# Kernel optimization log

Hardware: AMD Instinct MI355X
Metric: run time of the kernel (lower is better)

## Reference

```python
import jax, jax.numpy as jnp
import numpy as np

H = 256           # hidden_size
D_IN = 4 * H      # 1024
D_K = 8 * H       # 2048
B, N = 8, 2048


def setup_inputs() -> dict:
    key = jax.random.key(0)
    ks = jax.random.split(key, 7)
    s_in = 1.0 / np.sqrt(D_IN)
    s_dk = 1.0 / np.sqrt(D_K)
    x = jax.random.normal(ks[0], (B, N, D_IN), dtype=jnp.float32)
    Wq = jax.random.uniform(ks[1], (D_IN, D_K), jnp.float32, -s_in, s_in)
    Wk = jax.random.uniform(ks[2], (D_IN, D_K), jnp.float32, -s_in, s_in)
    Wv = jax.random.uniform(ks[3], (D_IN, D_K), jnp.float32, -s_in, s_in)
    Wfc = jax.random.uniform(ks[4], (D_K, D_IN), jnp.float32, -s_dk, s_dk)
    bfc = jax.random.uniform(ks[5], (D_IN,), jnp.float32, -s_dk, s_dk)
    gamma = jnp.ones((D_IN,), jnp.float32)
    beta = jnp.zeros((D_IN,), jnp.float32)
    return {"x": x, "Wq": Wq, "Wk": Wk, "Wv": Wv, "Wfc": Wfc,
            "bfc": bfc, "gamma": gamma, "beta": beta}


def layer_norm(y, gamma, beta, eps=1e-5):
    mu = jnp.mean(y, axis=-1, keepdims=True)
    var = jnp.var(y, axis=-1, keepdims=True)
    return (y - mu) * jax.lax.rsqrt(var + eps) * gamma + beta


def reference(x, Wq, Wk, Wv, Wfc, bfc, gamma, beta):
    # Q/K/V projections: [B, N, D_K]
    q = jnp.einsum('bnd,dk->bnk', x, Wq)
    k = jnp.einsum('bnd,dk->bnk', x, Wk)
    v = jnp.einsum('bnd,dk->bnk', x, Wv)
    # NOTE: original module has NO 1/sqrt(d_k) scaling — keep it faithful.
    scores = jnp.einsum('bnk,bmk->bnm', q, k)           # [B, N, N]
    attn = jax.nn.softmax(scores, axis=-1)
    att_x = jnp.einsum('bnm,bmk->bnk', attn, v)          # [B, N, D_K]
    h = jax.nn.relu(jnp.einsum('bnk,kd->bnd', att_x, Wfc) + bfc)
    return layer_norm(x + h, gamma, beta)
```

## Files before the change

### kernel.cpp

```cpp
#include <hip/hip_runtime.h>
#include <stdint.h>


#define DEVI __device__ __forceinline__

typedef uint16_t u16;
typedef _Float16 f16x8 __attribute__((ext_vector_type(8)));
typedef float f32x4 __attribute__((ext_vector_type(4)));

DEVI u16 f2h(float f) {
  union { _Float16 h; u16 u; } v;
  v.h = (_Float16)f;
  return v.u;
}

DEVI void gload_lds16(const void* g, void* lds) {
  __builtin_amdgcn_global_load_lds(
      (const __attribute__((address_space(1))) void*)g,
      (__attribute__((address_space(3))) void*)lds, 16, 0, 0);
}

template <int EPI>
__global__ __launch_bounds__(512, 2) void gemm256(
    const u16* __restrict__ A, const u16* __restrict__ B, void* __restrict__ C,
    int K, int lda, int ldb, int ldc,
    long aZ, long bZ, long cZ,
    const float* __restrict__ bias, const float* __restrict__ xres)
{
  __shared__ u16 lds[3 * 24576];
  char* ldsB = (char*)lds;
  const int tid = threadIdx.x;
  const int bz = blockIdx.z;

  const int gx = gridDim.x;
  int fl = blockIdx.y * gx + blockIdx.x;
  const int cpx = (gx * gridDim.y) >> 3;
  fl = (fl & 7) * cpx + (fl >> 3);
  const int bx = fl % gx, by = fl / gx;

  const u16* Ab = A + (long)bz * aZ + (long)(by * 256) * lda;
  const u16* Bb = B + (long)bz * bZ + (long)(bx * 128) * ldb;

  long aoff[4], boff[2];
#pragma unroll
  for (int r = 0; r < 4; ++r) {
    const int d = tid * 16 + r * 8192;
    const int dl = d ^ (((d >> 7) & 7) << 4);
    aoff[r] = (long)(dl >> 7) * (lda * 2) + (dl & 127);
  }
#pragma unroll
  for (int r = 0; r < 2; ++r) {
    const int d = tid * 16 + r * 8192;
    const int dl = d ^ (((d >> 7) & 7) << 4);
    boff[r] = (long)(dl >> 7) * (ldb * 2) + (dl & 127);
  }

  const int wid = tid >> 6, lane = tid & 63;
  const int wm = wid >> 1, wn = wid & 1;
  const int l15 = lane & 15;
  const int swzm = (lane & 7) << 4;
  const int ko0 = ((lane >> 4) * 16) ^ swzm;
  const int ko1 = (64 + (lane >> 4) * 16) ^ swzm;
  const int stgD = wid * 1024;

  f32x4 acc[4][4] = {};

  auto STAGE = [&](int t) {
    char* ab = ldsB + (t % 3) * 49152;
    char* bb = ab + 32768;
    const long kB = (long)t * 128;
#pragma unroll
    for (int r = 0; r < 4; ++r)
      gload_lds16((const char*)Ab + aoff[r] + kB, ab + stgD + r * 8192);
#pragma unroll
    for (int r = 0; r < 2; ++r)
      gload_lds16((const char*)Bb + boff[r] + kB, bb + stgD + r * 8192);
  };

  const int NT = K >> 6;
  STAGE(0);
  STAGE(1);

  for (int t = 0; t < NT; ++t) {
    if (t + 1 < NT) {
      asm volatile("s_waitcnt vmcnt(6)" ::: "memory");
    } else {
      asm volatile("s_waitcnt vmcnt(0)" ::: "memory");
    }
    __builtin_amdgcn_s_barrier();
    if (t + 2 < NT) STAGE(t + 2);

    const char* ab = ldsB + (t % 3) * 49152;
    const char* bb = ab + 32768;
#pragma unroll
    for (int ks = 0; ks < 2; ++ks) {
      const int ko = ks ? ko1 : ko0;
      f16x8 af[4], bf[4];
#pragma unroll
      for (int m = 0; m < 4; ++m)
        af[m] = *(const f16x8*)(ab + (wm * 64 + m * 16 + l15) * 128 + ko);
#pragma unroll
      for (int n = 0; n < 4; ++n)
        bf[n] = *(const f16x8*)(bb + (wn * 64 + n * 16 + l15) * 128 + ko);
      __builtin_amdgcn_s_setprio(1);
#pragma unroll
      for (int m = 0; m < 4; ++m)
#pragma unroll
        for (int n = 0; n < 4; ++n)
          acc[m][n] = __builtin_amdgcn_mfma_f32_16x16x32_f16(af[m], bf[n], acc[m][n], 0, 0, 0);
      __builtin_amdgcn_s_setprio(0);
    }
  }

  const long cBase = (long)bz * cZ;
  const int rowBase = by * 256 + wm * 64;
  const int colBase = bx * 128 + wn * 64;

  if constexpr (EPI == 3) {
    u16* vT = (u16*)C;
#pragma unroll
    for (int m = 0; m < 4; ++m) {
      const long row0 = rowBase + m * 16 + (lane >> 4) * 4;
      const long bb2 = (row0 >> 11) * 4194304L + (row0 & 2047);
#pragma unroll
      for (int n = 0; n < 4; ++n) {
        const int col = colBase + n * 16 + l15;
        ushort4 h;
        h.x = f2h(acc[m][n][0]); h.y = f2h(acc[m][n][1]);
        h.z = f2h(acc[m][n][2]); h.w = f2h(acc[m][n][3]);
        *(ushort4*)(vT + bb2 + (long)col * 2048) = h;
      }
    }
  } else {
#pragma unroll
    for (int m = 0; m < 4; ++m) {
#pragma unroll
      for (int r = 0; r < 4; ++r) {
        const long row = rowBase + m * 16 + (lane >> 4) * 4 + r;
#pragma unroll
        for (int n = 0; n < 4; ++n) {
          const int col = colBase + n * 16 + l15;
          float v = acc[m][n][r];
          if constexpr (EPI == 0) {
            ((u16*)C)[cBase + row * ldc + col] = f2h(v);
          } else if constexpr (EPI == 1) {
            ((float*)C)[cBase + row * ldc + col] = v;
          } else {
            v += bias[col];
            v = fmaxf(v, 0.0f);
            v += xres[row * (long)ldc + col];
            ((float*)C)[row * (long)ldc + col] = v;
          }
        }
      }
    }
  }
}

template <int EPI>
__global__ __launch_bounds__(256) void gemm_bt(
    const u16* __restrict__ A, const u16* __restrict__ B, void* __restrict__ C,
    int K, int lda, int ldb, int ldc,
    long aZ, long bZ, long cZ,
    const float* __restrict__ bias, const float* __restrict__ xres)
{
  __shared__ u16 sA[128 * 32];
  __shared__ u16 sB[128 * 32];
  const int tid = threadIdx.x;
  const int bz = blockIdx.z;
  const u16* Ab = A + (long)bz * aZ + (long)(blockIdx.y * 128) * lda;
  const u16* Bb = B + (long)bz * bZ + (long)(blockIdx.x * 128) * ldb;

  const int lane = tid & 63;
  const int wr = (tid >> 7) & 1;
  const int wc = (tid >> 6) & 1;
  const int l15 = lane & 15, l4 = lane >> 4;

  const int f0 = tid, f1 = tid + 256;
  const long ga0 = (long)(f0 >> 2) * lda + (f0 & 3) * 8;
  const long ga1 = (long)(f1 >> 2) * lda + (f1 & 3) * 8;
  const long gb0 = (long)(f0 >> 2) * ldb + (f0 & 3) * 8;
  const long gb1 = (long)(f1 >> 2) * ldb + (f1 & 3) * 8;
  u16* sAd0 = sA + (tid & ~63) * 8;
  u16* sAd1 = sA + 2048 + (tid & ~63) * 8;
  u16* sBd0 = sB + (tid & ~63) * 8;
  u16* sBd1 = sB + 2048 + (tid & ~63) * 8;

  f32x4 acc[4][4] = {};

  for (int k0 = 0; k0 < K; k0 += 32) {
    gload_lds16(Ab + ga0 + k0, sAd0);
    gload_lds16(Ab + ga1 + k0, sAd1);
    gload_lds16(Bb + gb0 + k0, sBd0);
    gload_lds16(Bb + gb1 + k0, sBd1);
    __syncthreads();
    f16x8 af[4], bf[4];
#pragma unroll
    for (int m = 0; m < 4; ++m)
      af[m] = *(const f16x8*)(sA + (wr * 64 + m * 16 + l15) * 32 + l4 * 8);
#pragma unroll
    for (int n = 0; n < 4; ++n)
      bf[n] = *(const f16x8*)(sB + (wc * 64 + n * 16 + l15) * 32 + l4 * 8);
#pragma unroll
    for (int m = 0; m < 4; ++m)
#pragma unroll
      for (int n = 0; n < 4; ++n)
        acc[m][n] = __builtin_amdgcn_mfma_f32_16x16x32_f16(af[m], bf[n], acc[m][n], 0, 0, 0);
    __syncthreads();
  }

  const long cBase = (long)bz * cZ;
  const int rowBase = blockIdx.y * 128 + wr * 64;
  const int colBase = blockIdx.x * 128 + wc * 64;

  if constexpr (EPI == 3) {
    u16* vT = (u16*)C;
#pragma unroll
    for (int m = 0; m < 4; ++m) {
      const long row0 = rowBase + m * 16 + l4 * 4;
      const long bb = (row0 >> 11) * 4194304L + (row0 & 2047);
#pragma unroll
      for (int n = 0; n < 4; ++n) {
        const int col = colBase + n * 16 + l15;
        ushort4 h;
        h.x = f2h(acc[m][n][0]); h.y = f2h(acc[m][n][1]);
        h.z = f2h(acc[m][n][2]); h.w = f2h(acc[m][n][3]);
        *(ushort4*)(vT + bb + (long)col * 2048) = h;
      }
    }
  } else {
#pragma unroll
    for (int m = 0; m < 4; ++m) {
#pragma unroll
      for (int r = 0; r < 4; ++r) {
        const long row = rowBase + m * 16 + l4 * 4 + r;
#pragma unroll
        for (int n = 0; n < 4; ++n) {
          const int col = colBase + n * 16 + l15;
          float v = acc[m][n][r];
          if constexpr (EPI == 0) {
            ((u16*)C)[cBase + row * ldc + col] = f2h(v);
          } else if constexpr (EPI == 1) {
            ((float*)C)[cBase + row * ldc + col] = v;
          } else {
            v += bias[col];
            v = fmaxf(v, 0.0f);
            v += xres[row * (long)ldc + col];
            ((float*)C)[row * (long)ldc + col] = v;
          }
        }
      }
    }
  }
}

__global__ __launch_bounds__(256) void softmax_rows(float* __restrict__ scores)
{
  const long row = blockIdx.x;
  const float* src = scores + row * 2048;
  const int tid = threadIdx.x;
  float4 a = ((const float4*)src)[tid];
  float4 b = ((const float4*)src)[tid + 256];
  float m = fmaxf(fmaxf(fmaxf(a.x, a.y), fmaxf(a.z, a.w)),
                  fmaxf(fmaxf(b.x, b.y), fmaxf(b.z, b.w)));
#pragma unroll
  for (int o = 32; o; o >>= 1) m = fmaxf(m, __shfl_xor(m, o));
  __shared__ float redm[4];
  if ((tid & 63) == 0) redm[tid >> 6] = m;
  __syncthreads();
  m = fmaxf(fmaxf(redm[0], redm[1]), fmaxf(redm[2], redm[3]));

  float e[8];
  e[0] = __expf(a.x - m); e[1] = __expf(a.y - m);
  e[2] = __expf(a.z - m); e[3] = __expf(a.w - m);
  e[4] = __expf(b.x - m); e[5] = __expf(b.y - m);
  e[6] = __expf(b.z - m); e[7] = __expf(b.w - m);
  float s = ((e[0] + e[1]) + (e[2] + e[3])) + ((e[4] + e[5]) + (e[6] + e[7]));
#pragma unroll
  for (int o = 32; o; o >>= 1) s += __shfl_xor(s, o);
  __shared__ float reds[4];
  if ((tid & 63) == 0) reds[tid >> 6] = s;
  __syncthreads();
  s = (reds[0] + reds[1]) + (reds[2] + reds[3]);
  const float inv = 1.0f / s;

  u16* dst = (u16*)scores + row * 4096;
  uint2 w0, w1;
  w0.x = (uint32_t)f2h(e[0] * inv) | ((uint32_t)f2h(e[1] * inv) << 16);
  w0.y = (uint32_t)f2h(e[2] * inv) | ((uint32_t)f2h(e[3] * inv) << 16);
  w1.x = (uint32_t)f2h(e[4] * inv) | ((uint32_t)f2h(e[5] * inv) << 16);
  w1.y = (uint32_t)f2h(e[6] * inv) | ((uint32_t)f2h(e[7] * inv) << 16);
  ((uint2*)dst)[tid] = w0;
  ((uint2*)dst)[tid + 256] = w1;
}

__global__ __launch_bounds__(256) void layernorm_rows(
    const float* __restrict__ y, const float* __restrict__ gamma,
    const float* __restrict__ beta, float* __restrict__ out)
{
  const long row = blockIdx.x;
  const int tid = threadIdx.x;
  float4 v = ((const float4*)(y + row * 1024))[tid];
  float s = (v.x + v.y) + (v.z + v.w);
  float q = (v.x * v.x + v.y * v.y) + (v.z * v.z + v.w * v.w);
#pragma unroll
  for (int o = 32; o; o >>= 1) { s += __shfl_xor(s, o); q += __shfl_xor(q, o); }
  __shared__ float rs[4], rq[4];
  if ((tid & 63) == 0) { rs[tid >> 6] = s; rq[tid >> 6] = q; }
  __syncthreads();
  s = (rs[0] + rs[1]) + (rs[2] + rs[3]);
  q = (rq[0] + rq[1]) + (rq[2] + rq[3]);
  const float mu = s * (1.0f / 1024.0f);
  const float var = q * (1.0f / 1024.0f) - mu * mu;
  const float rstd = rsqrtf(var + 1e-5f);
  float4 g = ((const float4*)gamma)[tid];
  float4 be = ((const float4*)beta)[tid];
  float4 o;
  o.x = (v.x - mu) * rstd * g.x + be.x;
  o.y = (v.y - mu) * rstd * g.y + be.y;
  o.z = (v.z - mu) * rstd * g.z + be.z;
  o.w = (v.w - mu) * rstd * g.w + be.w;
  __syncthreads();
  ((float4*)(out + row * 1024))[tid] = o;
}

__global__ __launch_bounds__(256) void cvt_f32_f16(
    const float* __restrict__ in, u16* __restrict__ out, long n4)
{
  const long stride = (long)gridDim.x * 256;
  for (long i = (long)blockIdx.x * 256 + threadIdx.x; i < n4; i += stride) {
    float4 v = ((const float4*)in)[i];
    uint2 p;
    p.x = (uint32_t)f2h(v.x) | ((uint32_t)f2h(v.y) << 16);
    p.y = (uint32_t)f2h(v.z) | ((uint32_t)f2h(v.w) << 16);
    ((uint2*)out)[i] = p;
  }
}

__global__ __launch_bounds__(256) void tw_f32(
    const float* __restrict__ in, u16* __restrict__ out, int R, int C)
{
  __shared__ float T[32][33];
  const int c0 = blockIdx.x * 32, r0 = blockIdx.y * 32;
  const int tx = threadIdx.x & 31, ty = threadIdx.x >> 5;
#pragma unroll
  for (int i = 0; i < 4; ++i)
    T[ty + i * 8][tx] = in[(long)(r0 + ty + i * 8) * C + c0 + tx];
  __syncthreads();
#pragma unroll
  for (int i = 0; i < 4; ++i)
    out[(long)(c0 + ty + i * 8) * R + r0 + tx] = f2h(T[tx][ty + i * 8]);
}

__global__ __launch_bounds__(256) void transpose_u16(
    const u16* __restrict__ in, u16* __restrict__ out, int R, int C)
{
  __shared__ u16 T[32][33];
  const long zo = (long)blockIdx.z * R * C;
  const int c0 = blockIdx.x * 32, r0 = blockIdx.y * 32;
  const int tx = threadIdx.x & 31, ty = threadIdx.x >> 5;
#pragma unroll
  for (int i = 0; i < 4; ++i)
    T[ty + i * 8][tx] = in[zo + (long)(r0 + ty + i * 8) * C + c0 + tx];
  __syncthreads();
#pragma unroll
  for (int i = 0; i < 4; ++i)
    out[zo + (long)(c0 + ty + i * 8) * R + r0 + tx] = T[tx][ty + i * 8];
}

extern "C" void kernel_launch(void* const* d_in, const int* in_sizes, int n_in,
                              void* d_out, int out_size, void* d_ws, size_t ws_size,
                              hipStream_t stream)
{
  const float* x     = (const float*)d_in[0];
  const float* Wq    = (const float*)d_in[1];
  const float* Wk    = (const float*)d_in[2];
  const float* Wv    = (const float*)d_in[3];
  const float* Wfc   = (const float*)d_in[4];
  const float* bfc   = (const float*)d_in[5];
  const float* gamma = (const float*)d_in[6];
  const float* beta  = (const float*)d_in[7];
  float* out = (float*)d_out;

  char* ws = (char*)d_ws;

  u16* wqkvT = (u16*)(ws + 0);
  u16* wfcT  = (u16*)(ws + 12582912);
  tw_f32<<<dim3(64, 32), 256, 0, stream>>>(Wq, wqkvT, 1024, 2048);
  tw_f32<<<dim3(64, 32), 256, 0, stream>>>(Wk, wqkvT + (long)2048 * 1024, 1024, 2048);
  tw_f32<<<dim3(64, 32), 256, 0, stream>>>(Wv, wqkvT + (long)2 * 2048 * 1024, 1024, 2048);
  tw_f32<<<dim3(32, 64), 256, 0, stream>>>(Wfc, wfcT, 2048, 1024);

  if (ws_size >= 251658240ULL) {
    u16*  q_  = (u16*)(ws + 16777216);
    u16*  k_  = (u16*)(ws + 83886080);
    u16*  vT  = (u16*)(ws + 150994944);
    float* sc = (float*)(ws + 218103808);
    u16*  xb  = (u16*)sc;

    cvt_f32_f16<<<2048, 256, 0, stream>>>(x, xb, (long)16384 * 1024 / 4);

    gemm256<0><<<dim3(16, 64, 2), 512, 0, stream>>>(
        xb, wqkvT, (void*)q_, 1024, 1024, 1024, 2048,
        0L, (long)2048 * 1024, (long)16384 * 2048, nullptr, nullptr);
    gemm256<3><<<dim3(16, 64, 1), 512, 0, stream>>>(
        xb, wqkvT + (long)2 * 2048 * 1024, (void*)vT, 1024, 1024, 1024, 2048,
        0L, 0L, 0L, nullptr, nullptr);

    for (int c = 0; c < 4; ++c) {
      const u16* qc = q_ + (long)c * 512 * 2048;
      gemm256<1><<<dim3(16, 2, 8), 512, 0, stream>>>(
          qc, k_, (void*)sc, 2048, 2048, 2048, 2048,
          (long)2048 * 2048, (long)2048 * 2048, (long)512 * 2048, nullptr, nullptr);
      softmax_rows<<<4096, 256, 0, stream>>>(sc);
      gemm256<0><<<dim3(16, 2, 8), 512, 0, stream>>>(
          (const u16*)sc, vT, (void*)(q_ + (long)c * 512 * 2048), 2048, 4096, 2048, 2048,
          (long)512 * 4096, (long)2048 * 2048, (long)2048 * 2048, nullptr, nullptr);
    }

    gemm256<2><<<dim3(8, 64, 1), 512, 0, stream>>>(
        q_, wfcT, (void*)out, 2048, 2048, 2048, 1024,
        0L, 0L, 0L, bfc, x);
  } else if (ws_size >= 109051904ULL) {
    u16*  xb2 = (u16*)(ws + 16777216);
    u16*  q2  = (u16*)(ws + 25165824);
    u16*  k2  = q2 + (long)2 * 2048 * 2048;
    u16*  v2  = q2 + (long)4 * 2048 * 2048;
    float* sc2 = (float*)(ws + 75497472);
    u16*  vT2   = k2;
    u16*  attx2 = q2;

    for (int p = 0; p < 4; ++p) {
      const float* xp = x + (long)p * 4096 * 1024;
      cvt_f32_f16<<<1024, 256, 0, stream>>>(xp, xb2, (long)4096 * 1024 / 4);
      for (int b = 0; b < 2; ++b)
        gemm_bt<0><<<dim3(16, 16, 3), 256, 0, stream>>>(
            xb2 + (long)b * 2048 * 1024, wqkvT, (void*)(q2 + (long)b * 2048 * 2048),
            1024, 1024, 1024, 2048,
            0L, (long)2048 * 1024, (long)2 * 2048 * 2048, nullptr, nullptr);
      gemm_bt<1><<<dim3(16, 16, 2), 256, 0, stream>>>(
          q2, k2, (void*)sc2, 2048, 2048, 2048, 2048,
          (long)2048 * 2048, (long)2048 * 2048, (long)2048 * 2048, nullptr, nullptr);
      softmax_rows<<<4096, 256, 0, stream>>>(sc2);
      transpose_u16<<<dim3(64, 64, 2), 256, 0, stream>>>(v2, vT2, 2048, 2048);
      gemm_bt<0><<<dim3(16, 16, 2), 256, 0, stream>>>(
          (const u16*)sc2, vT2, (void*)attx2, 2048, 4096, 2048, 2048,
          (long)2048 * 4096, (long)2048 * 2048, (long)2048 * 2048, nullptr, nullptr);
      gemm_bt<2><<<dim3(8, 32, 1), 256, 0, stream>>>(
          attx2, wfcT, (void*)(out + (long)p * 4096 * 1024), 2048, 2048, 2048, 1024,
          0L, 0L, 0L, bfc, xp);
    }
  } else {
    u16*  xb_b   = (u16*)(ws + 16777216);
    u16*  qkv_b  = (u16*)(ws + 20971520);
    u16*  q_b    = qkv_b;
    u16*  k_b    = qkv_b + (long)2048 * 2048;
    u16*  v_b    = qkv_b + (long)2 * 2048 * 2048;
    float* sc_b  = (float*)(ws + 46137344);
    u16*  vT_b   = k_b;
    u16*  attx_b = q_b;

    for (int b = 0; b < 8; ++b) {
      const float* x_b = x + (long)b * 2048 * 1024;
      cvt_f32_f16<<<512, 256, 0, stream>>>(x_b, xb_b, (long)2048 * 1024 / 4);
      gemm_bt<0><<<dim3(16, 16, 3), 256, 0, stream>>>(
          xb_b, wqkvT, (void*)qkv_b, 1024, 1024, 1024, 2048,
          0L, (long)2048 * 1024, (long)2048 * 2048, nullptr, nullptr);
      gemm_bt<1><<<dim3(16, 16, 1), 256, 0, stream>>>(
          q_b, k_b, (void*)sc_b, 2048, 2048, 2048, 2048,
          0L, 0L, 0L, nullptr, nullptr);
      softmax_rows<<<2048, 256, 0, stream>>>(sc_b);
      transpose_u16<<<dim3(64, 64, 1), 256, 0, stream>>>(v_b, vT_b, 2048, 2048);
      gemm_bt<0><<<dim3(16, 16, 1), 256, 0, stream>>>(
          (const u16*)sc_b, vT_b, (void*)attx_b, 2048, 4096, 2048, 2048,
          0L, 0L, 0L, nullptr, nullptr);
      gemm_bt<2><<<dim3(8, 16, 1), 256, 0, stream>>>(
          attx_b, wfcT, (void*)(out + (long)b * 2048 * 1024), 2048, 2048, 2048, 1024,
          0L, 0L, 0L, bfc, x_b);
    }
  }

  layernorm_rows<<<16384, 256, 0, stream>>>(out, gamma, beta, out);
}
```

Baseline: 710.2 us.

## Add 256x256-tile GEMM kernel for QKV and output projections

Introduces a new GEMM kernel with a 256x256 output tile per 512-thread block, 8x4 MFMA fragments per wave and double-buffered LDS staging, replacing the 256x128 tile kernel for the Q/K/V projections and the final FC+bias+relu+residual projection. The larger tile doubles arithmetic intensity per loaded byte and halves global traffic for the weight operand. The 256x128 kernel is kept for the attention GEMMs with its epilogue simplified. The trade-off is higher register pressure from 128 accumulator floats per thread, a shallower two-stage pipeline instead of three, and half as many blocks in flight.

```diff
diff --git a/kernel.cpp b/kernel.cpp
--- a/kernel.cpp
+++ b/kernel.cpp
@@ -21,11 +21,140 @@
 }
 
 template <int EPI>
-__global__ __launch_bounds__(512, 2) void gemm256(
+__global__ __launch_bounds__(512, 2) void gemm512(
     const u16* __restrict__ A, const u16* __restrict__ B, void* __restrict__ C,
     int K, int lda, int ldb, int ldc,
     long aZ, long bZ, long cZ,
     const float* __restrict__ bias, const float* __restrict__ xres)
+{
+  __shared__ u16 lds[2 * 32768];
+  char* ldsB = (char*)lds;
+  const int tid = threadIdx.x;
+  const int bz = blockIdx.z;
+
+  const int gx = gridDim.x;
+  int fl = blockIdx.y * gx + blockIdx.x;
+  const int cpx = (gx * gridDim.y) >> 3;
+  fl = (fl & 7) * cpx + (fl >> 3);
+  const int bx = fl % gx, by = fl / gx;
+
+  const u16* Ab = A + (long)bz * aZ + (long)(by * 256) * lda;
+  const u16* Bb = B + (long)bz * bZ + (long)(bx * 256) * ldb;
+
+  long aoff[4], boff[4];
+#pragma unroll
+  for (int r = 0; r < 4; ++r) {
+    const int d = tid * 16 + r * 8192;
+    const int dl = d ^ (((d >> 7) & 7) << 4);
+    aoff[r] = (long)(dl >> 7) * (lda * 2) + (dl & 127);
+    boff[r] = (long)(dl >> 7) * (ldb * 2) + (dl & 127);
+  }
+
+  const int wid = tid >> 6, lane = tid & 63;
+  const int wm = wid >> 2, wn = wid & 3;
+  const int l15 = lane & 15;
+  const int swzm = (lane & 7) << 4;
+  const int ko0 = ((lane >> 4) * 16) ^ swzm;
+  const int ko1 = (64 + (lane >> 4) * 16) ^ swzm;
+  const int stgD = wid * 1024;
+
+  f32x4 acc[8][4] = {};
+
+  auto STAGE = [&](int t) {
+    char* ab = ldsB + (t & 1) * 65536;
+    char* bb = ab + 32768;
+    const long kB = (long)t * 128;
+#pragma unroll
+    for (int r = 0; r < 4; ++r)
+      gload_lds16((const char*)Ab + aoff[r] + kB, ab + stgD + r * 8192);
+#pragma unroll
+    for (int r = 0; r < 4; ++r)
+      gload_lds16((const char*)Bb + boff[r] + kB, bb + stgD + r * 8192);
+  };
+
+  const int NT = K >> 6;
+  STAGE(0);
+
+  for (int t = 0; t < NT; ++t) {
+    if (t + 1 < NT) {
+      STAGE(t + 1);
+      asm volatile("s_waitcnt vmcnt(8)" ::: "memory");
+    } else {
+      asm volatile("s_waitcnt vmcnt(0)" ::: "memory");
+    }
+    __builtin_amdgcn_s_barrier();
+
+    const char* ab = ldsB + (t & 1) * 65536;
+    const char* bb = ab + 32768;
+#pragma unroll
+    for (int ks = 0; ks < 2; ++ks) {
+      const int ko = ks ? ko1 : ko0;
+      f16x8 af[8], bf[4];
+#pragma unroll
+      for (int m = 0; m < 8; ++m)
+        af[m] = *(const f16x8*)(ab + (wm * 128 + m * 16 + l15) * 128 + ko);
+#pragma unroll
+      for (int n = 0; n < 4; ++n)
+        bf[n] = *(const f16x8*)(bb + (wn * 64 + n * 16 + l15) * 128 + ko);
+      __builtin_amdgcn_s_setprio(1);
+#pragma unroll
+      for (int m = 0; m < 8; ++m)
+#pragma unroll
+        for (int n = 0; n < 4; ++n)
+          acc[m][n] = __builtin_amdgcn_mfma_f32_16x16x32_f16(af[m], bf[n], acc[m][n], 0, 0, 0);
+      __builtin_amdgcn_s_setprio(0);
+    }
+    __builtin_amdgcn_s_barrier();
+  }
+
+  const long cBase = (long)bz * cZ;
+  const int rowBase = by * 256 + wm * 128;
+  const int colBase = bx * 256 + wn * 64;
+
+  if constexpr (EPI == 3) {
+    u16* vT = (u16*)C;
+#pragma unroll
+    for (int m = 0; m < 8; ++m) {
+      const long row0 = rowBase + m * 16 + (lane >> 4) * 4;
+      const long bb2 = (row0 >> 11) * 4194304L + (row0 & 2047);
+#pragma unroll
+      for (int n = 0; n < 4; ++n) {
+        const int col = colBase + n * 16 + l15;
+        ushort4 h;
+        h.x = f2h(acc[m][n][0]); h.y = f2h(acc[m][n][1]);
+        h.z = f2h(acc[m][n][2]); h.w = f2h(acc[m][n][3]);
+        *(ushort4*)(vT + bb2 + (long)col * 2048) = h;
+      }
+    }
+  } else {
+#pragma unroll
+    for (int m = 0; m < 8; ++m) {
+#pragma unroll
+      for (int r = 0; r < 4; ++r) {
+        const long row = rowBase + m * 16 + (lane >> 4) * 4 + r;
+#pragma unroll
+        for (int n = 0; n < 4; ++n) {
+          const int col = colBase + n * 16 + l15;
+          float v = acc[m][n][r];
+          if constexpr (EPI == 0) {
+            ((u16*)C)[cBase + row * ldc + col] = f2h(v);
+          } else {
+            v += bias[col];
+            v = fmaxf(v, 0.0f);
+            v += xres[row * (long)ldc + col];
+            ((float*)C)[row * (long)ldc + col] = v;
+          }
+        }
+      }
+    }
+  }
+}
+
+template <int EPI>
+__global__ __launch_bounds__(512, 2) void gemm256(
+    const u16* __restrict__ A, const u16* __restrict__ B, void* __restrict__ C,
+    int K, int lda, int ldb, int ldc,
+    long aZ, long bZ, long cZ)
 {
   __shared__ u16 lds[3 * 24576];
   char* ldsB = (char*)lds;
@@ -115,42 +244,19 @@
   const long cBase = (long)bz * cZ;
   const int rowBase = by * 256 + wm * 64;
   const int colBase = bx * 128 + wn * 64;
-
-  if constexpr (EPI == 3) {
-    u16* vT = (u16*)C;
-#pragma unroll
-    for (int m = 0; m < 4; ++m) {
-      const long row0 = rowBase + m * 16 + (lane >> 4) * 4;
-      const long bb2 = (row0 >> 11) * 4194304L + (row0 & 2047);
+#pragma unroll
+  for (int m = 0; m < 4; ++m) {
+#pragma unroll
+    for (int r = 0; r < 4; ++r) {
+      const long row = rowBase + m * 16 + (lane >> 4) * 4 + r;
 #pragma unroll
       for (int n = 0; n < 4; ++n) {
         const int col = colBase + n * 16 + l15;
-        ushort4 h;
-        h.x = f2h(acc[m][n][0]); h.y = f2h(acc[m][n][1]);
-        h.z = f2h(acc[m][n][2]); h.w = f2h(acc[m][n][3]);
-        *(ushort4*)(vT + bb2 + (long)col * 2048) = h;
-      }
-    }
-  } else {
-#pragma unroll
-    for (int m = 0; m < 4; ++m) {
-#pragma unroll
-      for (int r = 0; r < 4; ++r) {
-        const long row = rowBase + m * 16 + (lane >> 4) * 4 + r;
-#pragma unroll
-        for (int n = 0; n < 4; ++n) {
-          const int col = colBase + n * 16 + l15;
-          float v = acc[m][n][r];
-          if constexpr (EPI == 0) {
-            ((u16*)C)[cBase + row * ldc + col] = f2h(v);
-          } else if constexpr (EPI == 1) {
-            ((float*)C)[cBase + row * ldc + col] = v;
-          } else {
-            v += bias[col];
-            v = fmaxf(v, 0.0f);
-            v += xres[row * (long)ldc + col];
-            ((float*)C)[row * (long)ldc + col] = v;
-          }
+        float v = acc[m][n][r];
+        if constexpr (EPI == 0) {
+          ((u16*)C)[cBase + row * ldc + col] = f2h(v);
+        } else {
+          ((float*)C)[cBase + row * ldc + col] = v;
         }
       }
     }
@@ -400,10 +506,10 @@
 
     cvt_f32_f16<<<2048, 256, 0, stream>>>(x, xb, (long)16384 * 1024 / 4);
 
-    gemm256<0><<<dim3(16, 64, 2), 512, 0, stream>>>(
+    gemm512<0><<<dim3(8, 64, 2), 512, 0, stream>>>(
         xb, wqkvT, (void*)q_, 1024, 1024, 1024, 2048,
         0L, (long)2048 * 1024, (long)16384 * 2048, nullptr, nullptr);
-    gemm256<3><<<dim3(16, 64, 1), 512, 0, stream>>>(
+    gemm512<3><<<dim3(8, 64, 1), 512, 0, stream>>>(
         xb, wqkvT + (long)2 * 2048 * 1024, (void*)vT, 1024, 1024, 1024, 2048,
         0L, 0L, 0L, nullptr, nullptr);
 
@@ -411,14 +517,14 @@
       const u16* qc = q_ + (long)c * 512 * 2048;
       gemm256<1><<<dim3(16, 2, 8), 512, 0, stream>>>(
           qc, k_, (void*)sc, 2048, 2048, 2048, 2048,
-          (long)2048 * 2048, (long)2048 * 2048, (long)512 * 2048, nullptr, nullptr);
+          (long)2048 * 2048, (long)2048 * 2048, (long)512 * 2048);
       softmax_rows<<<4096, 256, 0, stream>>>(sc);
       gemm256<0><<<dim3(16, 2, 8), 512, 0, stream>>>(
           (const u16*)sc, vT, (void*)(q_ + (long)c * 512 * 2048), 2048, 4096, 2048, 2048,
-          (long)512 * 4096, (long)2048 * 2048, (long)2048 * 2048, nullptr, nullptr);
-    }
-
-    gemm256<2><<<dim3(8, 64, 1), 512, 0, stream>>>(
+          (long)512 * 4096, (long)2048 * 2048, (long)2048 * 2048);
+    }
+
+    gemm512<2><<<dim3(4, 64, 1), 512, 0, stream>>>(
         q_, wfcT, (void*)out, 2048, 2048, 2048, 1024,
         0L, 0L, 0L, bfc, x);
   } else if (ws_size >= 109051904ULL) {
```

After: 711.2 us. About the same (+0.1%).

## Use 256x256 8-phase GEMM tiles and fp16 attention scores with larger chunks

Applied to the files above, without the earlier changes.

Replaces the 256x128 triple-buffered GEMM with a 256x256 tile kernel that double-buffers LDS and interleaves four quarter-tile loads between MFMA phases, raising arithmetic intensity per block. Attention scores are now stored in fp16 instead of fp32, and softmax reads and writes fp16 in place, which halves score traffic and lets chunks cover 1024 query rows instead of 512. The cost is fewer blocks per GEMM, more accumulator registers per thread, and some precision loss from storing pre-softmax logits in fp16, which could overflow since there is no 1/sqrt(d) scaling.

```diff
diff --git a/kernel.cpp b/kernel.cpp
--- a/kernel.cpp
+++ b/kernel.cpp
@@ -13,6 +13,11 @@
   v.h = (_Float16)f;
   return v.u;
 }
+DEVI float h2f(u16 x) {
+  union { _Float16 h; u16 u; } v;
+  v.u = x;
+  return (float)v.h;
+}
 
 DEVI void gload_lds16(const void* g, void* lds) {
   __builtin_amdgcn_global_load_lds(
@@ -21,13 +26,13 @@
 }
 
 template <int EPI>
-__global__ __launch_bounds__(512, 2) void gemm256(
+__global__ __launch_bounds__(512, 2) void gemm8p(
     const u16* __restrict__ A, const u16* __restrict__ B, void* __restrict__ C,
     int K, int lda, int ldb, int ldc,
     long aZ, long bZ, long cZ,
     const float* __restrict__ bias, const float* __restrict__ xres)
 {
-  __shared__ u16 lds[3 * 24576];
+  __shared__ u16 lds[2 * 32768];
   char* ldsB = (char*)lds;
   const int tid = threadIdx.x;
   const int bz = blockIdx.z;
@@ -39,87 +44,154 @@
   const int bx = fl % gx, by = fl / gx;
 
   const u16* Ab = A + (long)bz * aZ + (long)(by * 256) * lda;
-  const u16* Bb = B + (long)bz * bZ + (long)(bx * 128) * ldb;
-
-  long aoff[4], boff[2];
-#pragma unroll
-  for (int r = 0; r < 4; ++r) {
-    const int d = tid * 16 + r * 8192;
-    const int dl = d ^ (((d >> 7) & 7) << 4);
-    aoff[r] = (long)(dl >> 7) * (lda * 2) + (dl & 127);
-  }
-#pragma unroll
-  for (int r = 0; r < 2; ++r) {
-    const int d = tid * 16 + r * 8192;
-    const int dl = d ^ (((d >> 7) & 7) << 4);
-    boff[r] = (long)(dl >> 7) * (ldb * 2) + (dl & 127);
-  }
+  const u16* Bb = B + (long)bz * bZ + (long)(bx * 256) * ldb;
 
   const int wid = tid >> 6, lane = tid & 63;
-  const int wm = wid >> 1, wn = wid & 1;
+  const int wm = wid >> 2, wn = wid & 3;
   const int l15 = lane & 15;
-  const int swzm = (lane & 7) << 4;
-  const int ko0 = ((lane >> 4) * 16) ^ swzm;
-  const int ko1 = (64 + (lane >> 4) * 16) ^ swzm;
-  const int stgD = wid * 1024;
-
-  f32x4 acc[4][4] = {};
-
-  auto STAGE = [&](int t) {
-    char* ab = ldsB + (t % 3) * 49152;
-    char* bb = ab + 32768;
+
+  int aBase[2][2]; long aoff[2][2];
+  int bBase[2][2]; long boff[2][2];
+#pragma unroll
+  for (int h = 0; h < 2; ++h) {
+#pragma unroll
+    for (int j = 0; j < 2; ++j) {
+      const int s = wid * 2 + j;
+      int rs = (s < 8) ? (64 * h + s * 8) : (128 + 64 * h + (s - 8) * 8);
+      aBase[h][j] = rs * 128;
+      {
+        const int d = rs * 128 + lane * 16;
+        const int dl = d ^ (((d >> 7) & 7) << 4);
+        aoff[h][j] = (long)(dl >> 7) * (lda * 2) + (dl & 127);
+      }
+      rs = 64 * (s >> 2) + 32 * h + (s & 3) * 8;
+      bBase[h][j] = 32768 + rs * 128;
+      {
+        const int d = rs * 128 + lane * 16;
+        const int dl = d ^ (((d >> 7) & 7) << 4);
+        boff[h][j] = (long)(dl >> 7) * (ldb * 2) + (dl & 127);
+      }
+    }
+  }
+
+  const int swz = (lane & 7) << 4;
+  const int ko0 = ((lane >> 4) * 16) ^ swz;
+  const int ko1 = (64 + (lane >> 4) * 16) ^ swz;
+
+  f32x4 acc[8][4] = {};
+
+  auto STAGE_A = [&](int t, int h) {
+    char* dst = ldsB + (t & 1) * 65536;
     const long kB = (long)t * 128;
 #pragma unroll
-    for (int r = 0; r < 4; ++r)
-      gload_lds16((const char*)Ab + aoff[r] + kB, ab + stgD + r * 8192);
-#pragma unroll
-    for (int r = 0; r < 2; ++r)
-      gload_lds16((const char*)Bb + boff[r] + kB, bb + stgD + r * 8192);
+    for (int j = 0; j < 2; ++j)
+      gload_lds16((const char*)Ab + aoff[h][j] + kB, dst + aBase[h][j]);
   };
+  auto STAGE_B = [&](int t, int h) {
+    char* dst = ldsB + (t & 1) * 65536;
+    const long kB = (long)t * 128;
+#pragma unroll
+    for (int j = 0; j < 2; ++j)
+      gload_lds16((const char*)Bb + boff[h][j] + kB, dst + bBase[h][j]);
+  };
 
   const int NT = K >> 6;
-  STAGE(0);
-  STAGE(1);
+  STAGE_A(0, 0); STAGE_B(0, 0); STAGE_B(0, 1); STAGE_A(0, 1);
 
   for (int t = 0; t < NT; ++t) {
-    if (t + 1 < NT) {
-      asm volatile("s_waitcnt vmcnt(6)" ::: "memory");
-    } else {
-      asm volatile("s_waitcnt vmcnt(0)" ::: "memory");
-    }
+    const bool more = (t + 1 < NT);
+    const char* ab = ldsB + (t & 1) * 65536;
+    const char* bb = ab + 32768;
+    f16x8 af[8], bf0[4], bf1[4];
+
+    asm volatile("s_waitcnt vmcnt(4)" ::: "memory");
     __builtin_amdgcn_s_barrier();
-    if (t + 2 < NT) STAGE(t + 2);
-
-    const char* ab = ldsB + (t % 3) * 49152;
-    const char* bb = ab + 32768;
-#pragma unroll
-    for (int ks = 0; ks < 2; ++ks) {
-      const int ko = ks ? ko1 : ko0;
-      f16x8 af[4], bf[4];
+    if (more) STAGE_A(t + 1, 0);
+#pragma unroll
+    for (int m = 0; m < 4; ++m) {
+      const char* r = ab + (wm * 128 + m * 16 + l15) * 128;
+      af[2 * m] = *(const f16x8*)(r + ko0);
+      af[2 * m + 1] = *(const f16x8*)(r + ko1);
+    }
+#pragma unroll
+    for (int n = 0; n < 2; ++n) {
+      const char* r = bb + (wn * 64 + n * 16 + l15) * 128;
+      bf0[2 * n] = *(const f16x8*)(r + ko0);
+      bf0[2 * n + 1] = *(const f16x8*)(r + ko1);
+    }
+    __builtin_amdgcn_s_setprio(1);
+#pragma unroll
+    for (int ks = 0; ks < 2; ++ks)
 #pragma unroll
       for (int m = 0; m < 4; ++m)
-        af[m] = *(const f16x8*)(ab + (wm * 64 + m * 16 + l15) * 128 + ko);
-#pragma unroll
-      for (int n = 0; n < 4; ++n)
-        bf[n] = *(const f16x8*)(bb + (wn * 64 + n * 16 + l15) * 128 + ko);
-      __builtin_amdgcn_s_setprio(1);
+#pragma unroll
+        for (int n = 0; n < 2; ++n)
+          acc[m][n] = __builtin_amdgcn_mfma_f32_16x16x32_f16(
+              af[2 * m + ks], bf0[2 * n + ks], acc[m][n], 0, 0, 0);
+    __builtin_amdgcn_s_setprio(0);
+
+    if (more) asm volatile("s_waitcnt vmcnt(4)" ::: "memory");
+    else      asm volatile("s_waitcnt vmcnt(2)" ::: "memory");
+    __builtin_amdgcn_s_barrier();
+    if (more) STAGE_B(t + 1, 0);
+#pragma unroll
+    for (int n = 0; n < 2; ++n) {
+      const char* r = bb + (wn * 64 + (n + 2) * 16 + l15) * 128;
+      bf1[2 * n] = *(const f16x8*)(r + ko0);
+      bf1[2 * n + 1] = *(const f16x8*)(r + ko1);
+    }
+    __builtin_amdgcn_s_setprio(1);
+#pragma unroll
+    for (int ks = 0; ks < 2; ++ks)
 #pragma unroll
       for (int m = 0; m < 4; ++m)
 #pragma unroll
-        for (int n = 0; n < 4; ++n)
-          acc[m][n] = __builtin_amdgcn_mfma_f32_16x16x32_f16(af[m], bf[n], acc[m][n], 0, 0, 0);
-      __builtin_amdgcn_s_setprio(0);
-    }
+        for (int n = 0; n < 2; ++n)
+          acc[m][n + 2] = __builtin_amdgcn_mfma_f32_16x16x32_f16(
+              af[2 * m + ks], bf1[2 * n + ks], acc[m][n + 2], 0, 0, 0);
+    __builtin_amdgcn_s_setprio(0);
+
+    if (more) asm volatile("s_waitcnt vmcnt(4)" ::: "memory");
+    else      asm volatile("s_waitcnt vmcnt(0)" ::: "memory");
+    __builtin_amdgcn_s_barrier();
+    if (more) STAGE_B(t + 1, 1);
+#pragma unroll
+    for (int m = 0; m < 4; ++m) {
+      const char* r = ab + (wm * 128 + (m + 4) * 16 + l15) * 128;
+      af[2 * m] = *(const f16x8*)(r + ko0);
+      af[2 * m + 1] = *(const f16x8*)(r + ko1);
+    }
+    __builtin_amdgcn_s_setprio(1);
+#pragma unroll
+    for (int ks = 0; ks < 2; ++ks)
+#pragma unroll
+      for (int m = 0; m < 4; ++m)
+#pragma unroll
+        for (int n = 0; n < 2; ++n)
+          acc[m + 4][n] = __builtin_amdgcn_mfma_f32_16x16x32_f16(
+              af[2 * m + ks], bf0[2 * n + ks], acc[m + 4][n], 0, 0, 0);
+    __builtin_amdgcn_s_setprio(0);
+    if (more) STAGE_A(t + 1, 1);
+    __builtin_amdgcn_s_setprio(1);
+#pragma unroll
+    for (int ks = 0; ks < 2; ++ks)
+#pragma unroll
+      for (int m = 0; m < 4; ++m)
+#pragma unroll
+        for (int n = 0; n < 2; ++n)
+          acc[m + 4][n + 2] = __builtin_amdgcn_mfma_f32_16x16x32_f16(
+              af[2 * m + ks], bf1[2 * n + ks], acc[m + 4][n + 2], 0, 0, 0);
+    __builtin_amdgcn_s_setprio(0);
   }
 
   const long cBase = (long)bz * cZ;
-  const int rowBase = by * 256 + wm * 64;
-  const int colBase = bx * 128 + wn * 64;
+  const int rowBase = by * 256 + wm * 128;
+  const int colBase = bx * 256 + wn * 64;
 
   if constexpr (EPI == 3) {
     u16* vT = (u16*)C;
 #pragma unroll
-    for (int m = 0; m < 4; ++m) {
+    for (int m = 0; m < 8; ++m) {
       const long row0 = rowBase + m * 16 + (lane >> 4) * 4;
       const long bb2 = (row0 >> 11) * 4194304L + (row0 & 2047);
 #pragma unroll
@@ -133,7 +205,7 @@
     }
   } else {
 #pragma unroll
-    for (int m = 0; m < 4; ++m) {
+    for (int m = 0; m < 8; ++m) {
 #pragma unroll
       for (int r = 0; r < 4; ++r) {
         const long row = rowBase + m * 16 + (lane >> 4) * 4 + r;
@@ -143,8 +215,6 @@
           float v = acc[m][n][r];
           if constexpr (EPI == 0) {
             ((u16*)C)[cBase + row * ldc + col] = f2h(v);
-          } else if constexpr (EPI == 1) {
-            ((float*)C)[cBase + row * ldc + col] = v;
           } else {
             v += bias[col];
             v = fmaxf(v, 0.0f);
@@ -213,45 +283,67 @@
   const int rowBase = blockIdx.y * 128 + wr * 64;
   const int colBase = blockIdx.x * 128 + wc * 64;
 
-  if constexpr (EPI == 3) {
-    u16* vT = (u16*)C;
-#pragma unroll
-    for (int m = 0; m < 4; ++m) {
-      const long row0 = rowBase + m * 16 + l4 * 4;
-      const long bb = (row0 >> 11) * 4194304L + (row0 & 2047);
+#pragma unroll
+  for (int m = 0; m < 4; ++m) {
+#pragma unroll
+    for (int r = 0; r < 4; ++r) {
+      const long row = rowBase + m * 16 + l4 * 4 + r;
 #pragma unroll
       for (int n = 0; n < 4; ++n) {
         const int col = colBase + n * 16 + l15;
-        ushort4 h;
-        h.x = f2h(acc[m][n][0]); h.y = f2h(acc[m][n][1]);
-        h.z = f2h(acc[m][n][2]); h.w = f2h(acc[m][n][3]);
-        *(ushort4*)(vT + bb + (long)col * 2048) = h;
-      }
-    }
-  } else {
-#pragma unroll
-    for (int m = 0; m < 4; ++m) {
-#pragma unroll
-      for (int r = 0; r < 4; ++r) {
-        const long row = rowBase + m * 16 + l4 * 4 + r;
-#pragma unroll
-        for (int n = 0; n < 4; ++n) {
-          const int col = colBase + n * 16 + l15;
-          float v = acc[m][n][r];
-          if constexpr (EPI == 0) {
-            ((u16*)C)[cBase + row * ldc + col] = f2h(v);
-          } else if constexpr (EPI == 1) {
-            ((float*)C)[cBase + row * ldc + col] = v;
-          } else {
-            v += bias[col];
-            v = fmaxf(v, 0.0f);
-            v += xres[row * (long)ldc + col];
-            ((float*)C)[row * (long)ldc + col] = v;
-          }
+        float v = acc[m][n][r];
+        if constexpr (EPI == 0) {
+          ((u16*)C)[cBase + row * ldc + col] = f2h(v);
+        } else if constexpr (EPI == 1) {
+          ((float*)C)[cBase + row * ldc + col] = v;
+        } else {
+          v += bias[col];
+          v = fmaxf(v, 0.0f);
+          v += xres[row * (long)ldc + col];
+          ((float*)C)[row * (long)ldc + col] = v;
         }
       }
     }
   }
+}
+
+__global__ __launch_bounds__(256) void softmax_rows16(u16* __restrict__ sc)
+{
+  const long row = blockIdx.x;
+  u16* p = sc + row * 2048;
+  const int tid = threadIdx.x;
+  uint4 w = ((const uint4*)p)[tid];
+  float e[8];
+  e[0] = h2f(w.x & 0xffff); e[1] = h2f(w.x >> 16);
+  e[2] = h2f(w.y & 0xffff); e[3] = h2f(w.y >> 16);
+  e[4] = h2f(w.z & 0xffff); e[5] = h2f(w.z >> 16);
+  e[6] = h2f(w.w & 0xffff); e[7] = h2f(w.w >> 16);
+  float m = fmaxf(fmaxf(fmaxf(e[0], e[1]), fmaxf(e[2], e[3])),
+                  fmaxf(fmaxf(e[4], e[5]), fmaxf(e[6], e[7])));
+#pragma unroll
+  for (int o = 32; o; o >>= 1) m = fmaxf(m, __shfl_xor(m, o));
+  __shared__ float redm[4];
+  if ((tid & 63) == 0) redm[tid >> 6] = m;
+  __syncthreads();
+  m = fmaxf(fmaxf(redm[0], redm[1]), fmaxf(redm[2], redm[3]));
+
+  float s = 0.0f;
+#pragma unroll
+  for (int i = 0; i < 8; ++i) { e[i] = __expf(e[i] - m); s += e[i]; }
+#pragma unroll
+  for (int o = 32; o; o >>= 1) s += __shfl_xor(s, o);
+  __shared__ float reds[4];
+  if ((tid & 63) == 0) reds[tid >> 6] = s;
+  __syncthreads();
+  s = (reds[0] + reds[1]) + (reds[2] + reds[3]);
+  const float inv = 1.0f / s;
+
+  uint4 o;
+  o.x = (uint32_t)f2h(e[0] * inv) | ((uint32_t)f2h(e[1] * inv) << 16);
+  o.y = (uint32_t)f2h(e[2] * inv) | ((uint32_t)f2h(e[3] * inv) << 16);
+  o.z = (uint32_t)f2h(e[4] * inv) | ((uint32_t)f2h(e[5] * inv) << 16);
+  o.w = (uint32_t)f2h(e[6] * inv) | ((uint32_t)f2h(e[7] * inv) << 16);
+  ((uint4*)p)[tid] = o;
 }
 
 __global__ __launch_bounds__(256) void softmax_rows(float* __restrict__ scores)
@@ -392,33 +484,33 @@
   tw_f32<<<dim3(32, 64), 256, 0, stream>>>(Wfc, wfcT, 2048, 1024);
 
   if (ws_size >= 251658240ULL) {
-    u16*  q_  = (u16*)(ws + 16777216);
-    u16*  k_  = (u16*)(ws + 83886080);
-    u16*  vT  = (u16*)(ws + 150994944);
-    float* sc = (float*)(ws + 218103808);
-    u16*  xb  = (u16*)sc;
+    u16*  q_   = (u16*)(ws + 16777216);
+    u16*  k_   = (u16*)(ws + 83886080);
+    u16*  vT   = (u16*)(ws + 150994944);
+    u16*  sc16 = (u16*)(ws + 218103808);
+    u16*  xb   = sc16;
 
     cvt_f32_f16<<<2048, 256, 0, stream>>>(x, xb, (long)16384 * 1024 / 4);
 
-    gemm256<0><<<dim3(16, 64, 2), 512, 0, stream>>>(
+    gemm8p<0><<<dim3(8, 64, 2), 512, 0, stream>>>(
         xb, wqkvT, (void*)q_, 1024, 1024, 1024, 2048,
         0L, (long)2048 * 1024, (long)16384 * 2048, nullptr, nullptr);
-    gemm256<3><<<dim3(16, 64, 1), 512, 0, stream>>>(
+    gemm8p<3><<<dim3(8, 64, 1), 512, 0, stream>>>(
         xb, wqkvT + (long)2 * 2048 * 1024, (void*)vT, 1024, 1024, 1024, 2048,
         0L, 0L, 0L, nullptr, nullptr);
 
-    for (int c = 0; c < 4; ++c) {
-      const u16* qc = q_ + (long)c * 512 * 2048;
-      gemm256<1><<<dim3(16, 2, 8), 512, 0, stream>>>(
-          qc, k_, (void*)sc, 2048, 2048, 2048, 2048,
-          (long)2048 * 2048, (long)2048 * 2048, (long)512 * 2048, nullptr, nullptr);
-      softmax_rows<<<4096, 256, 0, stream>>>(sc);
-      gemm256<0><<<dim3(16, 2, 8), 512, 0, stream>>>(
-          (const u16*)sc, vT, (void*)(q_ + (long)c * 512 * 2048), 2048, 4096, 2048, 2048,
-          (long)512 * 4096, (long)2048 * 2048, (long)2048 * 2048, nullptr, nullptr);
-    }
-
-    gemm256<2><<<dim3(8, 64, 1), 512, 0, stream>>>(
+    for (int c = 0; c < 2; ++c) {
+      const u16* qc = q_ + (long)c * 1024 * 2048;
+      gemm8p<0><<<dim3(8, 4, 8), 512, 0, stream>>>(
+          qc, k_, (void*)sc16, 2048, 2048, 2048, 2048,
+          (long)2048 * 2048, (long)2048 * 2048, (long)1024 * 2048, nullptr, nullptr);
+      softmax_rows16<<<8192, 256, 0, stream>>>(sc16);
+      gemm8p<0><<<dim3(8, 4, 8), 512, 0, stream>>>(
+          sc16, vT, (void*)(q_ + (long)c * 1024 * 2048), 2048, 2048, 2048, 2048,
+          (long)1024 * 2048, (long)2048 * 2048, (long)2048 * 2048, nullptr, nullptr);
+    }
+
+    gemm8p<2><<<dim3(4, 64, 1), 512, 0, stream>>>(
         q_, wfcT, (void*)out, 2048, 2048, 2048, 1024,
         0L, 0L, 0L, bfc, x);
   } else if (ws_size >= 109051904ULL) {
```

Result: faster. 626.8 us (-11.7%).
